# Performance work log

Measured on AMD Instinct MI355X. Metric: run time of the kernel, lower is better.

The kernel has to match this reference:

```python
import jax, jax.numpy as jnp
import numpy as np
from jax import lax

KSIZE = 3      # match kernel
STRIDE = 1
RATE = 2       # dilation / downscale rate
FUSE_K = 3     # diagonal-fuse kernel
SCALE = 10.0   # softmax scale
FUSE = True
ESC = 1e-4     # escape_NaN, added per-element before the reduce_sum (as in torch code)


def _same_pad(x, k, s):
    # x: [C, H, W] -> zero-padded so that strided k-window 'same' extraction works
    C, H, W = x.shape
    oh, ow = -(-H // s), -(-W // s)
    ph = max(0, (oh - 1) * s + k - H)
    pw = max(0, (ow - 1) * s + k - W)
    xp = jnp.pad(x, ((0, 0), (ph // 2, ph - ph // 2), (pw // 2, pw - pw // 2)))
    return xp, oh, ow


def extract_patches(x, k, s):
    # x: [C, H, W] -> [L, C, k, k], L row-major over output grid (matches torch Unfold)
    C = x.shape[0]
    xp, oh, ow = _same_pad(x, k, s)
    cols = [xp[:, dh:dh + s * (oh - 1) + 1:s, dw:dw + s * (ow - 1) + 1:s]
            for dh in range(k) for dw in range(k)]
    p = jnp.stack(cols, 0).reshape(k, k, C, oh, ow)
    return p.transpose(3, 4, 2, 0, 1).reshape(oh * ow, C, k, k)


def fuse_diag(x):
    # conv with eye(FUSE_K) kernel, 'same' padding: sum of diagonal shifts
    A, B = x.shape
    pt = (FUSE_K - 1) // 2
    pb = FUSE_K - 1 - pt
    xp = jnp.pad(x, ((pt, pb), (pt, pb)))
    out = xp[0:A, 0:B]
    for d in range(1, FUSE_K):
        out = out + xp[d:d + A, d:d + B]
    return out


def _forward(f, b, mask):
    B, C, H, W = f.shape
    kernel = 2 * RATE
    # mask -> mm gate over background patches (shared across batch: torch uses m[0])
    mask_s = mask[0][:, ::4 * RATE, ::4 * RATE]           # [1, H/r, W/r] nearest downsample
    m = extract_patches(mask_s, KSIZE, STRIDE)            # [L, 1, k, k]
    mm = (jnp.mean(m, axis=(1, 2, 3)) == 0.0).astype(f.dtype)[:, None, None]  # [L,1,1]

    def single(fi, bi):
        # raw patches from full-res background for reconstruction: [Lb, C, 2r, 2r]
        raw_w = extract_patches(bi, kernel, RATE * STRIDE)
        # nearest 1/rate downsample
        fs = fi[:, ::RATE, ::RATE]
        bs = bi[:, ::RATE, ::RATE]
        bh, bw = bs.shape[1], bs.shape[2]
        fh, fw = fs.shape[1], fs.shape[2]
        Lb, Lf = bh * bw, fh * fw
        # match patches from downsampled background, L2-normalized per patch
        w = extract_patches(bs, KSIZE, STRIDE)                      # [Lb, C, 3, 3]
        denom = jnp.sqrt(jnp.sum(w * w + ESC, axis=(1, 2, 3), keepdims=True))
        wn = (w / denom).reshape(Lb, -1)                            # [Lb, C*9]
        # correlation = conv of fs with wn filters = patch GEMM
        fp = extract_patches(fs, KSIZE, 1).reshape(Lf, -1)          # [Lf, C*9]
        scores = wn @ fp.T                                          # [Lb, Lf]
        if FUSE:
            s = fuse_diag(scores)
            s = s.reshape(bh, bw, fh, fw).transpose(1, 0, 3, 2).reshape(Lb, Lf)
            s = fuse_diag(s)
            s = s.reshape(bw, bh, fw, fh).transpose(1, 0, 3, 2).reshape(Lb, Lf)
            scores = s
        att = scores.reshape(Lb, fh, fw) * mm
        att = jax.nn.softmax(att * SCALE, axis=0) * mm              # softmax over patches
        # conv_transpose2d(att, raw_w, stride=rate, padding=1) / 4
        rhs = jnp.flip(raw_w, (2, 3)).transpose(1, 0, 2, 3)         # [C, Lb, 2r, 2r] OIHW
        pad = kernel - 1 - 1                                        # k - 1 - torch_padding
        out = lax.conv_general_dilated(
            att[None], rhs, window_strides=(1, 1),
            padding=[(pad, pad), (pad, pad)], lhs_dilation=(RATE, RATE),
            dimension_numbers=('NCHW', 'OIHW', 'NCHW'))[0] / 4.0    # [C, H, W]
        return out

    return jax.vmap(single)(f, b)


def setup_inputs() -> dict:
    key = jax.random.key(0)
    k1, k2 = jax.random.split(key)
    B, C, H, W = 4, 128, 96, 96
    f = jax.random.normal(k1, (B, C, H, W), jnp.float32)
    b = jax.random.normal(k2, (B, C, H, W), jnp.float32)
    mask = jnp.zeros((1, 1, 4 * H, 4 * W), jnp.float32)
    mask = mask.at[:, :, 96:288, 96:288].set(1.0)
    return {"f": f, "b": b, "mask": mask}


def reference(f, b, mask):
    return _forward(f, b, mask)
```

## Files before the change

### kernel.cpp

```cpp
#include <hip/hip_runtime.h>

typedef _Float16 half8 __attribute__((ext_vector_type(8)));
typedef float floatx4 __attribute__((ext_vector_type(4)));

#define LBF 2304
#define K1  1152
#define LDK2 2304

__device__ __forceinline__ void gll16(const _Float16* g, _Float16* l) {
    __builtin_amdgcn_global_load_lds((const __attribute__((address_space(1))) void*)g,
                                     (__attribute__((address_space(3))) void*)l, 16, 0, 0);
}

__device__ __forceinline__ int dec_kc(int s) { return (s >= 0) ? s + 1 : -s - 1; }

__global__ __launch_bounds__(256)
void mask_scan(const float* __restrict__ mask, int* __restrict__ pos) {
    __shared__ float msk[48 * 48];
    int tid = threadIdx.x;
    for (int i = tid; i < 2304; i += 256) {
        int y = i / 48, x = i % 48;
        msk[i] = mask[(8 * y) * 384 + 8 * x];
    }
    __syncthreads();
    int mmb[9], loc[9]; int s = 0;
#pragma unroll
    for (int t = 0; t < 9; t++) {
        int p = tid * 9 + t;
        int pi = p / 48, pj = p % 48;
        float sm = 0.f;
#pragma unroll
        for (int u = 0; u < 3; u++)
#pragma unroll
            for (int v = 0; v < 3; v++) {
                int y = pi - 1 + u, x = pj - 1 + v;
                if ((unsigned)y < 48u && (unsigned)x < 48u)
                    sm += msk[y * 48 + x];
            }
        int m = (sm == 0.f) ? 1 : 0;
        mmb[t] = m; loc[t] = s; s += m;
    }
    __shared__ int sh[256];
    sh[tid] = s; __syncthreads();
    for (int off = 1; off < 256; off <<= 1) {
        int v = (tid >= off) ? sh[tid - off] : 0;
        __syncthreads();
        sh[tid] += v;
        __syncthreads();
    }
    int excl = sh[tid] - s;
#pragma unroll
    for (int t = 0; t < 9; t++) {
        int e = excl + loc[t];
        pos[tid * 9 + t] = mmb[t] ? e : (-e - 1);
    }
}

__global__ __launch_bounds__(256)
void prep_fw(const float* __restrict__ f, const float* __restrict__ bsrc,
             _Float16* __restrict__ fp, _Float16* __restrict__ wn) {
    int p = blockIdx.x, b = blockIdx.y;
    int pi = p / 48, pj = p % 48, tid = threadIdx.x;
    if (blockIdx.z == 0) {
        const float* fb = f + (long)b * 128 * 96 * 96;
        _Float16* orow = fp + ((long)b * LBF + p) * K1;
#pragma unroll
        for (int i = 0; i < 5; i++) {
            int k = tid + i * 256;
            if (k < K1) {
                int c = k / 9, r = k - 9 * c, u = r / 3, v = r - 3 * u;
                int y = pi - 1 + u, x = pj - 1 + v;
                float val = 0.f;
                if ((unsigned)y < 48u && (unsigned)x < 48u)
                    val = fb[(c * 96 + 2 * y) * 96 + 2 * x];
                orow[k] = (_Float16)val;
            }
        }
    } else {
        const float* bb = bsrc + (long)b * 128 * 96 * 96;
        _Float16* orow = wn + ((long)b * LBF + p) * K1;
        float w[5]; float ss = 0.f;
#pragma unroll
        for (int i = 0; i < 5; i++) {
            int k = tid + i * 256;
            float val = 0.f;
            if (k < K1) {
                int c = k / 9, r = k - 9 * c, u = r / 3, v = r - 3 * u;
                int y = pi - 1 + u, x = pj - 1 + v;
                if ((unsigned)y < 48u && (unsigned)x < 48u)
                    val = bb[(c * 96 + 2 * y) * 96 + 2 * x];
            }
            w[i] = val; ss += val * val;
        }
        for (int m = 32; m; m >>= 1) ss += __shfl_xor(ss, m);
        __shared__ float sh[4];
        if ((tid & 63) == 0) sh[tid >> 6] = ss;
        __syncthreads();
        float denom = sqrtf(sh[0] + sh[1] + sh[2] + sh[3] + 0.1152f);
        float inv = 1.f / denom;
#pragma unroll
        for (int i = 0; i < 5; i++) {
            int k = tid + i * 256;
            if (k < K1) orow[k] = (_Float16)(w[i] * inv);
        }
    }
}

__global__ void prep_wtc(const float* __restrict__ bsrc, const int* __restrict__ pos,
                         _Float16* __restrict__ wtc) {
    int p = blockIdx.x * 256 + threadIdx.x;
    int c = blockIdx.y;
    int b = blockIdx.z;
    int sp = pos[p];
    long base = ((long)b * 2048 + c * 16) * LDK2;
    if (sp < 0) {
        int kc = dec_kc(pos[2303]);
        int kp = (kc + 63) & ~63;
        int mo = p + sp + 1;
        if (mo < kp - kc) {
#pragma unroll
            for (int n = 0; n < 16; n++)
                wtc[base + (long)n * LDK2 + kc + mo] = (_Float16)0.f;
        }
        return;
    }
    int pi = p / 48, pj = p % 48;
    const float* src = bsrc + ((long)b * 128 + c) * 96 * 96;
#pragma unroll
    for (int u = 0; u < 4; u++) {
        int y = 2 * pi - 1 + u;
        bool yok = (unsigned)y < 96u;
#pragma unroll
        for (int v = 0; v < 4; v++) {
            int x = 2 * pj - 1 + v;
            float val = 0.f;
            if (yok && (unsigned)x < 96u) val = src[y * 96 + x];
            wtc[base + (long)(u * 4 + v) * LDK2 + sp] = (_Float16)val;
        }
    }
}

#define G1_REG 4096

__global__ __launch_bounds__(256)
void gemm1_cv(const _Float16* __restrict__ A, const _Float16* __restrict__ B,
              float* __restrict__ C) {
    __shared__ _Float16 SA[4 * G1_REG];
    __shared__ _Float16 SB[4 * G1_REG];

    int bid = blockIdx.x;
    int wg = (bid & 7) * 162 + (bid >> 3);
    int z = wg / 324; int t = wg - z * 324;
    const int m0 = (t / 18) * 128, n0 = (t % 18) * 128;

    const _Float16* gA = A + (long)z * LBF * K1 + (long)m0 * K1;
    const _Float16* gB = B + (long)z * LBF * K1 + (long)n0 * K1;
    float* Cb = C + (long)z * LBF * LBF;

    const int tid = threadIdx.x;
    const int wave = tid >> 6, lane = tid & 63;
    const int lm = lane & 15, q = lane >> 4;
    const int wm = wave >> 1, wn_ = wave & 1;
    const int soff = (q ^ ((lm >> 1) & 3)) * 8;
    const int srow = lane >> 2;
    const int scol = ((lane & 3) ^ ((lane >> 3) & 3)) * 8;

    floatx4 acc[4][4] = {};

    auto stA = [&](int reg, int kcol) {
        _Float16* dst = SA + reg * G1_REG + wave * 1024;
        gll16(gA + (long)(wave * 32 + srow) * K1 + kcol + scol, dst);
        gll16(gA + (long)(wave * 32 + 16 + srow) * K1 + kcol + scol, dst + 512);
    };
    auto stB = [&](int reg, int kcol) {
        _Float16* dst = SB + reg * G1_REG + wave * 1024;
        gll16(gB + (long)(wave * 32 + srow) * K1 + kcol + scol, dst);
        gll16(gB + (long)(wave * 32 + 16 + srow) * K1 + kcol + scol, dst + 512);
    };
    auto ldA = [&](int reg, int i) -> half8 {
        return *(const half8*)&SA[reg * G1_REG + (wm * 64 + i * 16 + lm) * 32 + soff];
    };
    auto ldB = [&](int reg, int j) -> half8 {
        return *(const half8*)&SB[reg * G1_REG + (wn_ * 64 + j * 16 + lm) * 32 + soff];
    };

    stA(0, 0);  stB(0, 0);
    stA(1, 32); stB(1, 32);
    stA(2, 64); stB(2, 64);
    asm volatile("s_waitcnt vmcnt(8)" ::: "memory");
    __builtin_amdgcn_s_barrier();
    __builtin_amdgcn_sched_barrier(0);

    for (int k = 0; k < 18; ++k) {
        const int b = k & 1;
        const int rg0 = b * 2, rg1 = rg0 + 1, og1 = (b ^ 1) * 2 + 1;
        {
            half8 af[4], bf[4];
#pragma unroll
            for (int i = 0; i < 4; ++i) af[i] = ldA(rg0, i);
#pragma unroll
            for (int j = 0; j < 4; ++j) bf[j] = ldB(rg0, j);
            if (k + 1 < 18) {
                int kc = (k + 1) * 64 + 32;
                stA(og1, kc); stB(og1, kc);
                asm volatile("s_waitcnt vmcnt(8) lgkmcnt(0)" ::: "memory");
            } else {
                asm volatile("s_waitcnt vmcnt(0) lgkmcnt(0)" ::: "memory");
            }
            __builtin_amdgcn_s_barrier();
            __builtin_amdgcn_sched_barrier(0);
            __builtin_amdgcn_s_setprio(1);
#pragma unroll
            for (int i = 0; i < 4; ++i)
#pragma unroll
                for (int j = 0; j < 4; ++j)
                    acc[i][j] = __builtin_amdgcn_mfma_f32_16x16x32_f16(af[i], bf[j], acc[i][j], 0, 0, 0);
            __builtin_amdgcn_s_setprio(0);
        }
        {
            half8 af[4], bf[4];
#pragma unroll
            for (int i = 0; i < 4; ++i) af[i] = ldA(rg1, i);
#pragma unroll
            for (int j = 0; j < 4; ++j) bf[j] = ldB(rg1, j);
            if (k + 2 < 18) {
                int kc = (k + 2) * 64;
                stA(rg0, kc); stB(rg0, kc);
                asm volatile("s_waitcnt vmcnt(8) lgkmcnt(0)" ::: "memory");
            } else {
                asm volatile("s_waitcnt vmcnt(0) lgkmcnt(0)" ::: "memory");
            }
            __builtin_amdgcn_s_barrier();
            __builtin_amdgcn_sched_barrier(0);
            __builtin_amdgcn_s_setprio(1);
#pragma unroll
            for (int i = 0; i < 4; ++i)
#pragma unroll
                for (int j = 0; j < 4; ++j)
                    acc[i][j] = __builtin_amdgcn_mfma_f32_16x16x32_f16(af[i], bf[j], acc[i][j], 0, 0, 0);
            __builtin_amdgcn_s_setprio(0);
        }
    }

    const int col = n0 + wn_ * 64 + lm;
#pragma unroll
    for (int i = 0; i < 4; ++i) {
        const int row = m0 + wm * 64 + i * 16 + q * 4;
#pragma unroll
        for (int j = 0; j < 4; ++j)
#pragma unroll
            for (int r = 0; r < 4; ++r)
                Cb[(long)(row + r) * LBF + col + j * 16] = acc[i][j][r];
    }
}

__device__ __forceinline__ void gemm_compute(const _Float16* lA, const _Float16* lB,
                                             floatx4 (&acc)[4][4],
                                             int wr, int wc, int lm, int pcp) {
    half8 af[4], bf[4];
#pragma unroll
    for (int t = 0; t < 4; t++) {
        af[t] = *(const half8*)&lA[(wr * 64 + t * 16 + lm) * 64 + pcp];
        bf[t] = *(const half8*)&lB[(wc * 64 + t * 16 + lm) * 64 + pcp];
    }
#pragma unroll
    for (int i = 0; i < 4; i++)
#pragma unroll
        for (int j = 0; j < 4; j++)
            acc[i][j] = __builtin_amdgcn_mfma_f32_16x16x32_f16(af[i], bf[j], acc[i][j], 0, 0, 0);
#pragma unroll
    for (int t = 0; t < 4; t++) {
        af[t] = *(const half8*)&lA[(wr * 64 + t * 16 + lm) * 64 + (pcp ^ 32)];
        bf[t] = *(const half8*)&lB[(wc * 64 + t * 16 + lm) * 64 + (pcp ^ 32)];
    }
#pragma unroll
    for (int i = 0; i < 4; i++)
#pragma unroll
        for (int j = 0; j < 4; j++)
            acc[i][j] = __builtin_amdgcn_mfma_f32_16x16x32_f16(af[i], bf[j], acc[i][j], 0, 0, 0);
}

__global__ __launch_bounds__(256)
void gemm_nt64(const _Float16* __restrict__ A, const _Float16* __restrict__ B,
               float* __restrict__ C, int M, int N, int ldk, int swapxy,
               const int* __restrict__ Kpos, int Kstat, long sA, long sB, long sC) {
    A += blockIdx.z * sA; B += blockIdx.z * sB; C += blockIdx.z * sC;
    int K;
    if (Kpos) { int kc = dec_kc(Kpos[0]); K = (kc + 63) & ~63; }
    else K = Kstat;
    const int tid = threadIdx.x;
    const int lane = tid & 63, wave = tid >> 6;
    const int wr = wave >> 1, wc = wave & 1;
    const int bm = swapxy ? blockIdx.x : blockIdx.y;
    const int bn = swapxy ? blockIdx.y : blockIdx.x;
    const int m0 = bm * 128, n0 = bn * 128;

    __shared__ _Float16 sm[4][128 * 64];

    floatx4 acc[4][4] = {};

    const int lm = lane & 15, q = lane >> 4;
    const int pcp = (q ^ (lm & 7)) * 8;

    const int srow8 = lane >> 3;
    const int gc = ((lane & 7) ^ srow8) * 8;
    const _Float16* gA[4]; const _Float16* gB[4];
    int dOff[4];
#pragma unroll
    for (int c = 0; c < 4; c++) {
        int r = (wave * 4 + c) * 8 + srow8;
        gA[c] = A + (long)(m0 + r) * ldk + gc;
        gB[c] = B + (long)(n0 + r) * ldk + gc;
        dOff[c] = (wave * 4 + c) * 512;
    }

    if (K > 0) {
#pragma unroll
        for (int c = 0; c < 4; c++) gll16(gA[c], &sm[0][dOff[c]]);
#pragma unroll
        for (int c = 0; c < 4; c++) gll16(gB[c], &sm[1][dOff[c]]);
        __syncthreads();
        int k0 = 0, buf = 0;
        while (true) {
            int kn = k0 + 64;
            if (kn < K) {
                const int nb = (buf ^ 1) * 2;
#pragma unroll
                for (int c = 0; c < 4; c++) gll16(gA[c] + kn, &sm[nb][dOff[c]]);
#pragma unroll
                for (int c = 0; c < 4; c++) gll16(gB[c] + kn, &sm[nb + 1][dOff[c]]);
            }
            gemm_compute(sm[buf * 2], sm[buf * 2 + 1], acc, wr, wc, lm, pcp);
            __syncthreads();
            k0 = kn; buf ^= 1;
            if (k0 >= K) break;
        }
    }

    const int col = n0 + wc * 64 + lm;
    const int rowq = q * 4;
#pragma unroll
    for (int i = 0; i < 4; i++) {
        int row = m0 + wr * 64 + i * 16 + rowq;
#pragma unroll
        for (int j = 0; j < 4; j++)
#pragma unroll
            for (int r = 0; r < 4; r++)
                C[(long)(row + r) * N + col + j * 16] = acc[i][j][r];
    }
}

__global__ __launch_bounds__(256)
void fuseA(const float* __restrict__ ST, float* __restrict__ FT1) {
    int y = blockIdx.x, bb = blockIdx.y;
    const float* S = ST + (long)bb * LBF * LBF;
    float* F = FT1 + (long)bb * LBF * LBF;
    const float* r0 = S + (long)(y > 0 ? y - 1 : 0) * LBF;
    const float* r1 = S + (long)y * LBF;
    const float* r2 = S + (long)(y < LBF - 1 ? y + 1 : y) * LBF;
    float m0 = (y > 0) ? 1.f : 0.f;
    float m2 = (y < LBF - 1) ? 1.f : 0.f;
    float* o = F + (long)y * LBF;
    int tid = threadIdx.x;
#pragma unroll
    for (int u = 0; u < 3; u++) {
        int qq = tid + u * 256;
        if (qq < LBF / 4) {
            int x0 = qq * 4;
            float4 a = *(const float4*)(r1 + x0);
            float4 b = *(const float4*)(r0 + x0);
            float4 c = *(const float4*)(r2 + x0);
            float lo_m1 = (x0 > 0) ? r0[x0 - 1] : 0.f;
            float hi_p4 = (x0 + 4 < LBF) ? r2[x0 + 4] : 0.f;
            float4 out;
            out.x = a.x + m0 * lo_m1 + m2 * c.y;
            out.y = a.y + m0 * b.x + m2 * c.z;
            out.z = a.z + m0 * b.y + m2 * c.w;
            out.w = a.w + m0 * b.z + m2 * hi_p4;
            *(float4*)(o + x0) = out;
        }
    }
}

__global__ __launch_bounds__(256)
void fuseB_softmax(const float* __restrict__ FT1, const int* __restrict__ pos,
                   _Float16* __restrict__ attTc_g) {
    int j = blockIdx.x, bb = blockIdx.y;
    int tid = threadIdx.x;
    const float* F = FT1 + (long)bb * LBF * LBF;
    _Float16* orow = attTc_g + ((long)bb * LBF + j) * LDK2;
    int Pj = (j % 48) * 48 + j / 48;
    long roff[3]; bool jok[3];
#pragma unroll
    for (int t = 0; t < 3; t++) {
        int j2 = Pj + t - 1;
        jok[t] = (unsigned)j2 < (unsigned)LBF;
        int jc = jok[t] ? j2 : 0;
        roff[t] = (long)((jc % 48) * 48 + jc / 48) * LBF;
    }
    float v[9]; int ps[9];
    float mx = -1e30f;
#pragma unroll
    for (int u = 0; u < 9; u++) {
        int x = tid + u * 256;
        int sp = pos[x];
        ps[u] = sp;
        float xv = 0.f;
        if (sp >= 0) {
            int a = x / 48, b = x - a * 48;
            int Px = b * 48 + a;
            float acc = 0.f;
#pragma unroll
            for (int t = 0; t < 3; t++) {
                int d2 = t - 1;
                int uu = Px + d2;
                if (jok[t] && (unsigned)uu < (unsigned)LBF) {
                    int ad = a + d2;
                    int c = ((unsigned)ad < 48u) ? (x + 48 * d2)
                          : (ad == 48 ? (b + 1) : (2255 + b));
                    acc += F[roff[t] + c];
                }
            }
            xv = acc * 10.f;
        }
        v[u] = xv;
        mx = fmaxf(mx, xv);
    }
    for (int m = 32; m; m >>= 1) mx = fmaxf(mx, __shfl_xor(mx, m));
    __shared__ float sh[4], sh2[4];
    if ((tid & 63) == 0) sh[tid >> 6] = mx;
    __syncthreads();
    mx = fmaxf(fmaxf(sh[0], sh[1]), fmaxf(sh[2], sh[3]));
    float sum = 0.f;
#pragma unroll
    for (int u = 0; u < 9; u++) { v[u] = __expf(v[u] - mx); sum += v[u]; }
    for (int m = 32; m; m >>= 1) sum += __shfl_xor(sum, m);
    if ((tid & 63) == 0) sh2[tid >> 6] = sum;
    __syncthreads();
    sum = sh2[0] + sh2[1] + sh2[2] + sh2[3];
    float inv = 1.f / sum;
#pragma unroll
    for (int u = 0; u < 9; u++) {
        if (ps[u] >= 0) orow[ps[u]] = (_Float16)(v[u] * inv);
    }
    int kc = dec_kc(pos[2303]);
    int kp = (kc + 63) & ~63;
    if (tid < kp - kc) orow[kc + tid] = (_Float16)0.f;
}

__global__ void scatter_out(const float* __restrict__ MT_, float* __restrict__ out) {
    int yx = blockIdx.x * 256 + threadIdx.x;
    int c = blockIdx.y, b = blockIdx.z;
    int y = yx / 96, x = yx % 96;
    const float* Mb = MT_ + (long)b * 2048 * LBF;
    float s = 0.f;
    for (int uu = (y + 1) & 1; uu < 4; uu += 2) {
        int fi = (y + 1 - uu) >> 1;
        if ((unsigned)fi >= 48u) continue;
        for (int vv = (x + 1) & 1; vv < 4; vv += 2) {
            int fj = (x + 1 - vv) >> 1;
            if ((unsigned)fj >= 48u) continue;
            s += Mb[(long)(c * 16 + uu * 4 + vv) * LBF + fi * 48 + fj];
        }
    }
    out[(((long)b * 128 + c) * 96 + y) * 96 + x] = 0.25f * s;
}

extern "C" void kernel_launch(void* const* d_in, const int* in_sizes, int n_in,
                              void* d_out, int out_size, void* d_ws, size_t ws_size,
                              hipStream_t stream) {
    const float* f    = (const float*)d_in[0];
    const float* bsrc = (const float*)d_in[1];
    const float* mask = (const float*)d_in[2];
    float* out = (float*)d_out;

    char* ws = (char*)d_ws;
    const size_t offR1  = 84934656;
    const size_t offWn  = offR1 + 21233664;
    const size_t offWtc = offR1 + 42467328;
    const size_t offFT1 = offWtc + 37748736;
    const size_t offPos = offFT1 + 2ul * 21233664;
    const size_t NEED   = offPos + 9216;
    if (ws_size < NEED) return;

    float*    ST    = (float*)(ws + 0);
    float*    MT    = (float*)(ws + 0);
    _Float16* fp    = (_Float16*)(ws + offR1);
    _Float16* wn    = (_Float16*)(ws + offWn);
    _Float16* attTc = (_Float16*)(ws + offR1);
    _Float16* Wtc   = (_Float16*)(ws + offWtc);
    float*    FT1   = (float*)(ws + offFT1);
    int*      pos   = (int*)(ws + offPos);

    mask_scan<<<dim3(1), 256, 0, stream>>>(mask, pos);
    prep_fw<<<dim3(2304, 4, 2), 256, 0, stream>>>(f, bsrc, fp, wn);
    prep_wtc<<<dim3(9, 128, 4), 256, 0, stream>>>(bsrc, pos, Wtc);

    gemm1_cv<<<dim3(1296), 256, 0, stream>>>(fp, wn, ST);

    for (int g = 0; g < 2; g++) {
        fuseA<<<dim3(LBF, 2), 256, 0, stream>>>(ST + (long)g * 2 * LBF * LBF, FT1);
        fuseB_softmax<<<dim3(LBF, 2), 256, 0, stream>>>(FT1, pos,
            attTc + (long)g * 2 * LBF * LDK2);
    }

    gemm_nt64<<<dim3(16, 18, 4), 256, 0, stream>>>(Wtc, attTc, MT, 2048, 2304, LDK2, 1,
        pos + 2303, 0, (long)2048 * LDK2, (long)2304 * LDK2, (long)2048 * 2304);

    scatter_out<<<dim3(36, 128, 4), 256, 0, stream>>>(MT, out);
}
```

Baseline: 442.1 us.

## Vectorize prep stores, fuse two rows per fuseA block, split GEMMs by batch

```diff
diff --git a/kernel.cpp b/kernel.cpp
--- a/kernel.cpp
+++ b/kernel.cpp
@@ -1,6 +1,7 @@
 #include <hip/hip_runtime.h>
 
 typedef _Float16 half8 __attribute__((ext_vector_type(8)));
+typedef _Float16 half4v __attribute__((ext_vector_type(4)));
 typedef float floatx4 __attribute__((ext_vector_type(4)));
 
 #define LBF 2304
@@ -65,32 +66,43 @@
         const float* fb = f + (long)b * 128 * 96 * 96;
         _Float16* orow = fp + ((long)b * LBF + p) * K1;
 #pragma unroll
-        for (int i = 0; i < 5; i++) {
-            int k = tid + i * 256;
-            if (k < K1) {
-                int c = k / 9, r = k - 9 * c, u = r / 3, v = r - 3 * u;
-                int y = pi - 1 + u, x = pj - 1 + v;
-                float val = 0.f;
-                if ((unsigned)y < 48u && (unsigned)x < 48u)
-                    val = fb[(c * 96 + 2 * y) * 96 + 2 * x];
-                orow[k] = (_Float16)val;
+        for (int i = 0; i < 2; i++) {
+            int qi = tid + i * 256;
+            if (qi < 288) {
+                int k0 = qi * 4;
+                half4v o;
+#pragma unroll
+                for (int e = 0; e < 4; e++) {
+                    int k = k0 + e;
+                    int c = k / 9, r = k - 9 * c, u = r / 3, v = r - 3 * u;
+                    int y = pi - 1 + u, x = pj - 1 + v;
+                    float val = 0.f;
+                    if ((unsigned)y < 48u && (unsigned)x < 48u)
+                        val = fb[(c * 96 + 2 * y) * 96 + 2 * x];
+                    o[e] = (_Float16)val;
+                }
+                *(half4v*)(orow + k0) = o;
             }
         }
     } else {
         const float* bb = bsrc + (long)b * 128 * 96 * 96;
         _Float16* orow = wn + ((long)b * LBF + p) * K1;
-        float w[5]; float ss = 0.f;
-#pragma unroll
-        for (int i = 0; i < 5; i++) {
-            int k = tid + i * 256;
-            float val = 0.f;
-            if (k < K1) {
-                int c = k / 9, r = k - 9 * c, u = r / 3, v = r - 3 * u;
-                int y = pi - 1 + u, x = pj - 1 + v;
-                if ((unsigned)y < 48u && (unsigned)x < 48u)
-                    val = bb[(c * 96 + 2 * y) * 96 + 2 * x];
-            }
-            w[i] = val; ss += val * val;
+        float w[2][4]; float ss = 0.f;
+#pragma unroll
+        for (int i = 0; i < 2; i++) {
+            int qi = tid + i * 256;
+#pragma unroll
+            for (int e = 0; e < 4; e++) {
+                float val = 0.f;
+                if (qi < 288) {
+                    int k = qi * 4 + e;
+                    int c = k / 9, r = k - 9 * c, u = r / 3, v = r - 3 * u;
+                    int y = pi - 1 + u, x = pj - 1 + v;
+                    if ((unsigned)y < 48u && (unsigned)x < 48u)
+                        val = bb[(c * 96 + 2 * y) * 96 + 2 * x];
+                }
+                w[i][e] = val; ss += val * val;
+            }
         }
         for (int m = 32; m; m >>= 1) ss += __shfl_xor(ss, m);
         __shared__ float sh[4];
@@ -99,9 +111,14 @@
         float denom = sqrtf(sh[0] + sh[1] + sh[2] + sh[3] + 0.1152f);
         float inv = 1.f / denom;
 #pragma unroll
-        for (int i = 0; i < 5; i++) {
-            int k = tid + i * 256;
-            if (k < K1) orow[k] = (_Float16)(w[i] * inv);
+        for (int i = 0; i < 2; i++) {
+            int qi = tid + i * 256;
+            if (qi < 288) {
+                half4v o;
+#pragma unroll
+                for (int e = 0; e < 4; e++) o[e] = (_Float16)(w[i][e] * inv);
+                *(half4v*)(orow + qi * 4) = o;
+            }
         }
     }
 }
@@ -144,13 +161,13 @@
 
 __global__ __launch_bounds__(256)
 void gemm1_cv(const _Float16* __restrict__ A, const _Float16* __restrict__ B,
-              float* __restrict__ C) {
+              float* __restrict__ C, int zoff) {
     __shared__ _Float16 SA[4 * G1_REG];
     __shared__ _Float16 SB[4 * G1_REG];
 
     int bid = blockIdx.x;
-    int wg = (bid & 7) * 162 + (bid >> 3);
-    int z = wg / 324; int t = wg - z * 324;
+    int wg = (bid & 7) * 81 + (bid >> 3);
+    int z = zoff + wg / 324; int t = wg % 324;
     const int m0 = (t / 18) * 128, n0 = (t % 18) * 128;
 
     const _Float16* gA = A + (long)z * LBF * K1 + (long)m0 * K1;
@@ -283,8 +300,10 @@
 __global__ __launch_bounds__(256)
 void gemm_nt64(const _Float16* __restrict__ A, const _Float16* __restrict__ B,
                float* __restrict__ C, int M, int N, int ldk, int swapxy,
-               const int* __restrict__ Kpos, int Kstat, long sA, long sB, long sC) {
-    A += blockIdx.z * sA; B += blockIdx.z * sB; C += blockIdx.z * sC;
+               const int* __restrict__ Kpos, int Kstat, long sA, long sB, long sC,
+               int zoff) {
+    int zz = blockIdx.z + zoff;
+    A += zz * sA; B += zz * sB; C += zz * sC;
     int K;
     if (Kpos) { int kc = dec_kc(Kpos[0]); K = (kc + 63) & ~63; }
     else K = Kstat;
@@ -352,32 +371,42 @@
 
 __global__ __launch_bounds__(256)
 void fuseA(const float* __restrict__ ST, float* __restrict__ FT1) {
-    int y = blockIdx.x, bb = blockIdx.y;
+    int y0 = blockIdx.x * 2, bb = blockIdx.y;
     const float* S = ST + (long)bb * LBF * LBF;
     float* F = FT1 + (long)bb * LBF * LBF;
-    const float* r0 = S + (long)(y > 0 ? y - 1 : 0) * LBF;
-    const float* r1 = S + (long)y * LBF;
-    const float* r2 = S + (long)(y < LBF - 1 ? y + 1 : y) * LBF;
-    float m0 = (y > 0) ? 1.f : 0.f;
-    float m2 = (y < LBF - 1) ? 1.f : 0.f;
-    float* o = F + (long)y * LBF;
+    const float* rm1 = S + (long)(y0 > 0 ? y0 - 1 : 0) * LBF;
+    const float* r0  = S + (long)y0 * LBF;
+    const float* r1  = S + (long)(y0 + 1) * LBF;
+    const float* r2  = S + (long)(y0 + 2 < LBF ? y0 + 2 : y0 + 1) * LBF;
+    float mA = (y0 > 0) ? 1.f : 0.f;
+    float mB = (y0 + 2 < LBF) ? 1.f : 0.f;
+    float* o0 = F + (long)y0 * LBF;
+    float* o1 = F + (long)(y0 + 1) * LBF;
     int tid = threadIdx.x;
 #pragma unroll
     for (int u = 0; u < 3; u++) {
         int qq = tid + u * 256;
         if (qq < LBF / 4) {
             int x0 = qq * 4;
-            float4 a = *(const float4*)(r1 + x0);
-            float4 b = *(const float4*)(r0 + x0);
-            float4 c = *(const float4*)(r2 + x0);
-            float lo_m1 = (x0 > 0) ? r0[x0 - 1] : 0.f;
-            float hi_p4 = (x0 + 4 < LBF) ? r2[x0 + 4] : 0.f;
-            float4 out;
-            out.x = a.x + m0 * lo_m1 + m2 * c.y;
-            out.y = a.y + m0 * b.x + m2 * c.z;
-            out.z = a.z + m0 * b.y + m2 * c.w;
-            out.w = a.w + m0 * b.z + m2 * hi_p4;
-            *(float4*)(o + x0) = out;
+            float4 vm1 = *(const float4*)(rm1 + x0);
+            float4 v0  = *(const float4*)(r0 + x0);
+            float4 v1  = *(const float4*)(r1 + x0);
+            float4 v2  = *(const float4*)(r2 + x0);
+            float lo0 = (x0 > 0) ? rm1[x0 - 1] : 0.f;
+            float lo1 = (x0 > 0) ? r0[x0 - 1] : 0.f;
+            float hi0 = (x0 + 4 < LBF) ? r1[x0 + 4] : 0.f;
+            float hi1 = (x0 + 4 < LBF) ? r2[x0 + 4] : 0.f;
+            float4 out0, out1;
+            out0.x = v0.x + mA * lo0   + v1.y;
+            out0.y = v0.y + mA * vm1.x + v1.z;
+            out0.z = v0.z + mA * vm1.y + v1.w;
+            out0.w = v0.w + mA * vm1.z + hi0;
+            out1.x = v1.x + lo1  + mB * v2.y;
+            out1.y = v1.y + v0.x + mB * v2.z;
+            out1.z = v1.z + v0.y + mB * v2.w;
+            out1.w = v1.w + v0.z + mB * hi1;
+            *(float4*)(o0 + x0) = out0;
+            *(float4*)(o1 + x0) = out1;
         }
     }
 }
@@ -496,16 +525,19 @@
     prep_fw<<<dim3(2304, 4, 2), 256, 0, stream>>>(f, bsrc, fp, wn);
     prep_wtc<<<dim3(9, 128, 4), 256, 0, stream>>>(bsrc, pos, Wtc);
 
-    gemm1_cv<<<dim3(1296), 256, 0, stream>>>(fp, wn, ST);
+    gemm1_cv<<<dim3(648), 256, 0, stream>>>(fp, wn, ST, 0);
+    gemm1_cv<<<dim3(648), 256, 0, stream>>>(fp, wn, ST, 2);
 
     for (int g = 0; g < 2; g++) {
-        fuseA<<<dim3(LBF, 2), 256, 0, stream>>>(ST + (long)g * 2 * LBF * LBF, FT1);
+        fuseA<<<dim3(LBF / 2, 2), 256, 0, stream>>>(ST + (long)g * 2 * LBF * LBF, FT1);
         fuseB_softmax<<<dim3(LBF, 2), 256, 0, stream>>>(FT1, pos,
             attTc + (long)g * 2 * LBF * LDK2);
     }
 
-    gemm_nt64<<<dim3(16, 18, 4), 256, 0, stream>>>(Wtc, attTc, MT, 2048, 2304, LDK2, 1,
-        pos + 2303, 0, (long)2048 * LDK2, (long)2304 * LDK2, (long)2048 * 2304);
+    gemm_nt64<<<dim3(16, 18, 2), 256, 0, stream>>>(Wtc, attTc, MT, 2048, 2304, LDK2, 1,
+        pos + 2303, 0, (long)2048 * LDK2, (long)2304 * LDK2, (long)2048 * 2304, 0);
+    gemm_nt64<<<dim3(16, 18, 2), 256, 0, stream>>>(Wtc, attTc, MT, 2048, 2304, LDK2, 1,
+        pos + 2303, 0, (long)2048 * LDK2, (long)2304 * LDK2, (long)2048 * 2304, 2);
 
     scatter_out<<<dim3(36, 128, 4), 256, 0, stream>>>(MT, out);
 }
```

New measurement: 497.2 us. 12.5% more time.
